# Kernel optimization log

Measured on AMD Instinct MI355X. Metric: run time of the kernel, lower is better.

The kernel has to match this reference:

```python
import jax, jax.numpy as jnp
import numpy as np

DIM_MODEL = 1024
HEADS = 16
DIM_PER_HEAD = DIM_MODEL // HEADS


def setup_inputs() -> dict:
    key = jax.random.key(0)
    k0, k1, k2, k3, k4 = jax.random.split(key, 5)
    x = jax.random.normal(k0, (2, 2048, DIM_MODEL), dtype=jnp.float32)
    # combined_linear: dim_model -> 3*dim_model (torch Linear: y = x @ W.T + b)
    s_in = 1.0 / np.sqrt(DIM_MODEL)
    W_qkv = jax.random.uniform(k1, (3 * DIM_MODEL, DIM_MODEL), minval=-s_in, maxval=s_in, dtype=jnp.float32)
    b_qkv = jax.random.uniform(k2, (3 * DIM_MODEL,), minval=-s_in, maxval=s_in, dtype=jnp.float32)
    W_out = jax.random.uniform(k3, (DIM_MODEL, DIM_MODEL), minval=-s_in, maxval=s_in, dtype=jnp.float32)
    b_out = jax.random.uniform(k4, (DIM_MODEL,), minval=-s_in, maxval=s_in, dtype=jnp.float32)
    return {"x": x, "W_qkv": W_qkv, "b_qkv": b_qkv, "W_out": W_out, "b_out": b_out}


def reference(x, W_qkv, b_qkv, W_out, b_out):
    B, S, D = x.shape
    H, Dh = HEADS, DIM_PER_HEAD
    qkv = x @ W_qkv.T + b_qkv  # [B, S, 3D]
    q, k, v = jnp.split(qkv, 3, axis=2)
    # [B, H, S, Dh]
    q = q.reshape(B, S, H, Dh).transpose(0, 2, 1, 3)
    k = k.reshape(B, S, H, Dh).transpose(0, 2, 1, 3)
    v = v.reshape(B, S, H, Dh).transpose(0, 2, 1, 3)
    scores = jnp.einsum('bhqd,bhkd->bhqk', q, k) / jnp.sqrt(jnp.float32(Dh))
    causal = jnp.tril(jnp.ones((S, S), dtype=bool))
    scores = jnp.where(causal[None, None, :, :], scores, -jnp.inf)
    p_attn = jax.nn.softmax(scores, axis=-1)
    out = jnp.einsum('bhqk,bhkd->bhqd', p_attn, v)
    out = out.transpose(0, 2, 1, 3).reshape(B, S, D)
    return out @ W_out.T + b_out
```

## Files before the change

kernel.cpp:

```cpp
#include <hip/hip_runtime.h>
#include <cstdint>

typedef __attribute__((ext_vector_type(8))) __bf16 bf16x8;
typedef __attribute__((ext_vector_type(4))) float f32x4;
typedef __attribute__((ext_vector_type(8))) short short8;
typedef __attribute__((ext_vector_type(4))) float float4v;
typedef __attribute__((ext_vector_type(4))) unsigned uint4v;
typedef __attribute__((ext_vector_type(4))) unsigned short ushort4v;

__device__ __forceinline__ unsigned short f2bf(float f) {
    unsigned u = __builtin_bit_cast(unsigned, f);
    u += 0x7fffu + ((u >> 16) & 1u);
    return (unsigned short)(u >> 16);
}
__device__ __forceinline__ float bf2f(unsigned short s) {
    return __builtin_bit_cast(float, (unsigned)s << 16);
}
__device__ __forceinline__ f32x4 mfma_bf16(bf16x8 a, bf16x8 b, f32x4 c) {
    return __builtin_amdgcn_mfma_f32_16x16x32_bf16(a, b, c, 0, 0, 0);
}
__device__ __forceinline__ unsigned pkbf(float lo, float hi) {
    unsigned r;
    asm("v_cvt_pk_bf16_f32 %0, %1, %2" : "=v"(r) : "v"(lo), "v"(hi));
    return r;
}

#define GLD16(g, l)                                                                     \
    __builtin_amdgcn_global_load_lds((const __attribute__((address_space(1))) void*)(g), \
                                     (__attribute__((address_space(3))) void*)(l), 16, 0, 0)

__global__ void __launch_bounds__(256) cvt_f32_bf16(const float* __restrict__ src,
                                                    unsigned short* __restrict__ dst, int n8) {
    const int stride = gridDim.x * blockDim.x;
    for (int i = blockIdx.x * blockDim.x + threadIdx.x; i < n8; i += stride) {
        const float4v* s = (const float4v*)(src + (size_t)i * 8);
        float4v v0 = s[0], v1 = s[1];
        short8 o;
        o[0] = (short)f2bf(v0[0]); o[1] = (short)f2bf(v0[1]);
        o[2] = (short)f2bf(v0[2]); o[3] = (short)f2bf(v0[3]);
        o[4] = (short)f2bf(v1[0]); o[5] = (short)f2bf(v1[1]);
        o[6] = (short)f2bf(v1[2]); o[7] = (short)f2bf(v1[3]);
        *(short8*)(dst + (size_t)i * 8) = o;
    }
}

template <int MODE>
__global__ void __launch_bounds__(256) gemm_bt(const unsigned short* __restrict__ A,
                                               const unsigned short* __restrict__ B,
                                               const float* __restrict__ bias,
                                               void* __restrict__ C,
                                               unsigned short* __restrict__ vT,
                                               int M, int N, int K) {
    __shared__ __attribute__((aligned(16))) unsigned short As[2][128 * 32];
    __shared__ __attribute__((aligned(16))) unsigned short Bs[2][128 * 32];
    const int tid = threadIdx.x;
    const int w = tid >> 6, lane = tid & 63;
    const int a = lane & 15, g = lane >> 4;
    const int m0 = blockIdx.y * 128, n0 = blockIdx.x * 128;
    const int wr = (w >> 1) * 64, wc = (w & 1) * 64;

    f32x4 acc[4][4];
#pragma unroll
    for (int i = 0; i < 4; i++)
#pragma unroll
        for (int j = 0; j < 4; j++) acc[i][j] = (f32x4)(0.0f);

    const int r0 = tid >> 2;
    const int c0 = (tid & 3) * 8;
    const unsigned short* gA0 = A + (size_t)(m0 + r0) * K + c0;
    const unsigned short* gA1 = A + (size_t)(m0 + 64 + r0) * K + c0;
    const unsigned short* gB0 = B + (size_t)(n0 + r0) * K + c0;
    const unsigned short* gB1 = B + (size_t)(n0 + 64 + r0) * K + c0;

#define GSTAGE(buf_, k0_)                                               \
    {                                                                   \
        char* la_ = (char*)&As[buf_][0] + w * 1024;                     \
        char* lb_ = (char*)&Bs[buf_][0] + w * 1024;                     \
        GLD16(gA0 + (k0_), la_);                                        \
        GLD16(gA1 + (k0_), la_ + 4096);                                 \
        GLD16(gB0 + (k0_), lb_);                                        \
        GLD16(gB1 + (k0_), lb_ + 4096);                                 \
    }

    GSTAGE(0, 0);
    __syncthreads();

    int cur = 0;
    for (int k0 = 0; k0 < K; k0 += 32) {
        if (k0 + 32 < K) GSTAGE(cur ^ 1, k0 + 32);

        bf16x8 af[4], bfr[4];
#pragma unroll
        for (int i = 0; i < 4; i++) {
            af[i]  = *(const bf16x8*)&As[cur][(wr + i * 16 + a) * 32 + g * 8];
            bfr[i] = *(const bf16x8*)&Bs[cur][(wc + i * 16 + a) * 32 + g * 8];
        }
#pragma unroll
        for (int i = 0; i < 4; i++)
#pragma unroll
            for (int j = 0; j < 4; j++) acc[i][j] = mfma_bf16(af[i], bfr[j], acc[i][j]);

        __syncthreads();
        cur ^= 1;
    }
#undef GSTAGE

#pragma unroll
    for (int j = 0; j < 4; j++) {
        const int col = n0 + wc + j * 16 + a;
        const float bv = bias[col];
        if (MODE == 0) {
            float* Cf = (float*)C;
#pragma unroll
            for (int i = 0; i < 4; i++)
#pragma unroll
                for (int jr = 0; jr < 4; jr++) {
                    const int row = m0 + wr + i * 16 + g * 4 + jr;
                    Cf[(size_t)row * N + col] = acc[i][j][jr] + bv;
                }
        } else if (n0 < 2048) {
            unsigned short* Cb = (unsigned short*)C;
#pragma unroll
            for (int i = 0; i < 4; i++)
#pragma unroll
                for (int jr = 0; jr < 4; jr++) {
                    const int row = m0 + wr + i * 16 + g * 4 + jr;
                    Cb[(size_t)row * 2048 + col] = f2bf(acc[i][j][jr] + bv);
                }
        } else {
            const int vd = col - 2048;
            const int hh = vd >> 6, dd = vd & 63;
#pragma unroll
            for (int i = 0; i < 4; i++) {
                const int token0 = m0 + wr + i * 16 + g * 4;
                const int bb = token0 >> 11, kl = token0 & 2047;
                ushort4v st;
#pragma unroll
                for (int jr = 0; jr < 4; jr++) st[jr] = f2bf(acc[i][j][jr] + bv);
                *(ushort4v*)(vT + ((size_t)((bb << 4) + hh) * 64 + dd) * 2048 + kl) = st;
            }
        }
    }
}


#define QKT_LDS(p, kvb)                                                 \
    {                                                                   \
        _Pragma("unroll") for (int nf_ = 0; nf_ < 4; nf_++) {           \
            const int r_ = srow + ((nf_ & 2) << 4) + ((nf_ & 1) << 2);  \
            const bf16x8 ka_ = *(const bf16x8*)&(kvb)[r_ * 64 + offKA]; \
            const bf16x8 kc_ = *(const bf16x8*)&(kvb)[r_ * 64 + offKB]; \
            f32x4 acc_ = (f32x4)(0.0f);                                 \
            acc_ = mfma_bf16(ka_, qf[0], acc_);                         \
            acc_ = mfma_bf16(kc_, qf[1], acc_);                         \
            p[nf_] = acc_;                                              \
        }                                                               \
    }

#define DIAG_MASK(p, qs_, k0_)                                          \
    {                                                                   \
        _Pragma("unroll") for (int nf_ = 0; nf_ < 4; nf_++) {           \
            const int kb_ = (k0_) + ((nf_ & 2) << 4) + ((nf_ & 1) << 2) + 8 * g; \
            _Pragma("unroll") for (int e_ = 0; e_ < 4; e_++)            \
                if (kb_ + e_ > (qs_)) p[nf_][e_] = -1e30f;              \
        }                                                               \
    }

#define SOFTMAX_PACK(p, m_, l_, of_, pf0, pf1)                          \
    {                                                                   \
        float x0 = fmaxf(fmaxf(p[0][0], p[0][1]), fmaxf(p[0][2], p[0][3])); \
        float x1 = fmaxf(fmaxf(p[1][0], p[1][1]), fmaxf(p[1][2], p[1][3])); \
        float x2 = fmaxf(fmaxf(p[2][0], p[2][1]), fmaxf(p[2][2], p[2][3])); \
        float x3 = fmaxf(fmaxf(p[3][0], p[3][1]), fmaxf(p[3][2], p[3][3])); \
        float mx = fmaxf(fmaxf(x0, x1), fmaxf(x2, x3));                 \
        mx = fmaxf(mx, __shfl_xor(mx, 16));                             \
        mx = fmaxf(mx, __shfl_xor(mx, 32));                             \
        if (!__all(mx <= m_ + 8.0f)) {                                  \
            const float mn_ = fmaxf(m_, mx);                            \
            const float al_ = __builtin_amdgcn_exp2f(m_ - mn_);         \
            l_ *= al_;                                                  \
            _Pragma("unroll") for (int d_ = 0; d_ < 4; d_++) of_[d_] = of_[d_] * al_; \
            m_ = mn_;                                                   \
        }                                                               \
        float rs_ = 0.0f;                                               \
        _Pragma("unroll") for (int nf_ = 0; nf_ < 4; nf_++)             \
            _Pragma("unroll") for (int e_ = 0; e_ < 4; e_++) {          \
                p[nf_][e_] = __builtin_amdgcn_exp2f(p[nf_][e_] - m_);   \
                rs_ += p[nf_][e_];                                      \
            }                                                           \
        l_ += rs_;                                                      \
        uint4v u0_, u1_;                                                \
        u0_[0] = pkbf(p[0][0], p[0][1]); u0_[1] = pkbf(p[0][2], p[0][3]); \
        u0_[2] = pkbf(p[1][0], p[1][1]); u0_[3] = pkbf(p[1][2], p[1][3]); \
        u1_[0] = pkbf(p[2][0], p[2][1]); u1_[1] = pkbf(p[2][2], p[2][3]); \
        u1_[2] = pkbf(p[3][0], p[3][1]); u1_[3] = pkbf(p[3][2], p[3][3]); \
        pf0 = __builtin_bit_cast(bf16x8, u0_);                          \
        pf1 = __builtin_bit_cast(bf16x8, u1_);                          \
    }

#define PV_LDS(of_, pf0, pf1, vb)                                       \
    {                                                                   \
        _Pragma("unroll") for (int df_ = 0; df_ < 4; df_++) {           \
            const bf16x8 va_ = *(const bf16x8*)&(vb)[(df_ * 16 + n) * 64 + offVA]; \
            const bf16x8 vc_ = *(const bf16x8*)&(vb)[(df_ * 16 + n) * 64 + offVB]; \
            of_[df_] = mfma_bf16(va_, pf0, of_[df_]);                   \
            of_[df_] = mfma_bf16(vc_, pf1, of_[df_]);                   \
        }                                                               \
    }

#define STAGE(bf_, t_)                                                  \
    {                                                                   \
        const size_t ko_ = (size_t)(t_) * 64 * LDQ;                     \
        const size_t vo_ = (size_t)(t_) * 64;                           \
        char* db_ = (char*)&KV[bf_][0] + w * 1024;                      \
        GLD16(sK0 + ko_, db_);                                          \
        GLD16(sV0 + vo_, db_ + 8192);                                   \
    }

__global__ void __launch_bounds__(512) attn_fwd(const unsigned short* __restrict__ qk,
                                                const unsigned short* __restrict__ vT,
                                                unsigned short* __restrict__ o) {
    constexpr int SL = 2048, DH = 64, LDQ = 2048;
    constexpr float GAMMA = 0.18033688011112042f;
    const int bh = blockIdx.x & 31;
    const int pr = 15 - (blockIdx.x >> 5);
    const int b = bh >> 4, h = bh & 15;
    const int tid = threadIdx.x;
    const int w = tid >> 6, lane = tid & 63;
    const int n = lane & 15, g = lane >> 4;

    __shared__ __attribute__((aligned(16))) unsigned short KV[2][8192];

    const int myqt = 2 * pr + (w >> 2);
    const int qs = myqt * 64 + (w & 3) * 16 + n;
    const int nt = 2 * pr + 2;

    bf16x8 qf[2];
    {
        const unsigned short* qp = qk + (size_t)(b * SL + qs) * LDQ + h * DH + g * 8;
        short8 la = *(const short8*)qp, lb = *(const short8*)(qp + 32);
        short8 s0, s1;
#pragma unroll
        for (int e = 0; e < 8; e++) {
            s0[e] = (short)f2bf(bf2f((unsigned short)la[e]) * GAMMA);
            s1[e] = (short)f2bf(bf2f((unsigned short)lb[e]) * GAMMA);
        }
        qf[0] = __builtin_bit_cast(bf16x8, s0);
        qf[1] = __builtin_bit_cast(bf16x8, s1);
    }

    const int r0s = tid >> 3, u0s = tid & 7;
    const int xrs = (r0s & 3) | (((r0s >> 3) & 1) << 2);
    const int cs = ((u0s ^ xrs) << 3);
    const unsigned short* sK0 = qk + (size_t)(b * SL + r0s) * LDQ + 1024 + h * DH + cs;
    const unsigned short* sV0 = vT + (size_t)bh * DH * SL + (size_t)r0s * SL + cs;

    const int srow = 8 * (n >> 2) + (n & 3);
    const int xrq = (n & 3) | (((n >> 2) & 1) << 2);
    const int offKA = ((g ^ xrq) << 3);
    const int offKB = offKA ^ 32;
    const int xrv = (n & 3) | (((n >> 3) & 1) << 2);
    const int offVA = ((g ^ xrv) << 3);
    const int offVB = offVA ^ 32;

    f32x4 of[4];
#pragma unroll
    for (int i = 0; i < 4; i++) of[i] = (f32x4)(0.0f);
    float m_i = -1e30f, l_i = 0.0f;

    STAGE(0, 0);
    __syncthreads();

    for (int t = 0; t < nt; ++t) {
        const unsigned short* kvb = &KV[t & 1][0];
        if (t + 1 < nt) STAGE((t & 1) ^ 1, t + 1);

        f32x4 p[4];
        QKT_LDS(p, kvb);
        if (t >= myqt) DIAG_MASK(p, qs, t * 64);
        bf16x8 f0, f1;
        SOFTMAX_PACK(p, m_i, l_i, of, f0, f1);
        PV_LDS(of, f0, f1, (kvb + 4096));

        __syncthreads();
    }

    float rl = l_i;
    rl += __shfl_xor(rl, 16);
    rl += __shfl_xor(rl, 32);
    const float inv = 1.0f / rl;
    unsigned short* op = o + (size_t)(b * SL + qs) * 1024 + h * DH + 4 * g;
#pragma unroll
    for (int df = 0; df < 4; df++) {
        ushort4v st;
#pragma unroll
        for (int r = 0; r < 4; r++) st[r] = f2bf(of[df][r] * inv);
        *(ushort4v*)(op + df * 16) = st;
    }
}

extern "C" void kernel_launch(void* const* d_in, const int* in_sizes, int n_in,
                              void* d_out, int out_size, void* d_ws, size_t ws_size,
                              hipStream_t stream) {
    (void)in_sizes; (void)n_in; (void)out_size; (void)ws_size;
    const float* x    = (const float*)d_in[0];
    const float* Wqkv = (const float*)d_in[1];
    const float* bqkv = (const float*)d_in[2];
    const float* Wout = (const float*)d_in[3];
    const float* bout = (const float*)d_in[4];
    float* out = (float*)d_out;

    const int BS = 2, SL = 2048, DM = 1024;
    const int M = BS * SL;
    const int N1 = 3 * DM;
    const int K = DM;

    char* ws = (char*)d_ws;
    unsigned short* x_bf    = (unsigned short*)(ws);
    unsigned short* wqkv_bf = (unsigned short*)(ws + (8u << 20));
    unsigned short* wout_bf = (unsigned short*)(ws + (14u << 20));
    unsigned short* qkbuf   = (unsigned short*)(ws + (16u << 20));
    unsigned short* vTbuf   = (unsigned short*)(ws + (32u << 20));
    unsigned short* attn_o  = (unsigned short*)(ws + (40u << 20));

    cvt_f32_bf16<<<2048, 256, 0, stream>>>(x, x_bf, M * K / 8);
    cvt_f32_bf16<<<1536, 256, 0, stream>>>(Wqkv, wqkv_bf, N1 * K / 8);
    cvt_f32_bf16<<<512, 256, 0, stream>>>(Wout, wout_bf, DM * DM / 8);

    gemm_bt<1><<<dim3(N1 / 128, M / 128), 256, 0, stream>>>(x_bf, wqkv_bf, bqkv, qkbuf, vTbuf, M, N1, K);

    attn_fwd<<<dim3(512), 512, 0, stream>>>(qkbuf, vTbuf, attn_o);

    gemm_bt<0><<<dim3(DM / 128, M / 128), 256, 0, stream>>>(attn_o, wout_bf, bout, out, nullptr, M, DM, K);
}
```

Measured before the change: 113.6 us.

## Process 128-key tiles with 128-query blocks in causal attention kernel

The attention kernel now gives each block 128 queries (one 16-row slice per wave) and iterates over 128-key K/V tiles instead of 64. This halves the number of loop iterations and __syncthreads barriers and doubles the work per staged LDS buffer. The block scheduling order becomes an interleave of long and short query blocks, and launch bounds request 4 blocks per CU. In exchange it uses twice the shared memory per block (64 KB) and more registers for the larger score tile. Causal masking now runs only on the final tile, where that tile is partly masked for most queries.

```diff
diff --git a/kernel.cpp b/kernel.cpp
--- a/kernel.cpp
+++ b/kernel.cpp
@@ -144,96 +144,34 @@
 }
 
 
-#define QKT_LDS(p, kvb)                                                 \
-    {                                                                   \
-        _Pragma("unroll") for (int nf_ = 0; nf_ < 4; nf_++) {           \
-            const int r_ = srow + ((nf_ & 2) << 4) + ((nf_ & 1) << 2);  \
-            const bf16x8 ka_ = *(const bf16x8*)&(kvb)[r_ * 64 + offKA]; \
-            const bf16x8 kc_ = *(const bf16x8*)&(kvb)[r_ * 64 + offKB]; \
-            f32x4 acc_ = (f32x4)(0.0f);                                 \
-            acc_ = mfma_bf16(ka_, qf[0], acc_);                         \
-            acc_ = mfma_bf16(kc_, qf[1], acc_);                         \
-            p[nf_] = acc_;                                              \
-        }                                                               \
-    }
-
-#define DIAG_MASK(p, qs_, k0_)                                          \
-    {                                                                   \
-        _Pragma("unroll") for (int nf_ = 0; nf_ < 4; nf_++) {           \
-            const int kb_ = (k0_) + ((nf_ & 2) << 4) + ((nf_ & 1) << 2) + 8 * g; \
-            _Pragma("unroll") for (int e_ = 0; e_ < 4; e_++)            \
-                if (kb_ + e_ > (qs_)) p[nf_][e_] = -1e30f;              \
-        }                                                               \
-    }
-
-#define SOFTMAX_PACK(p, m_, l_, of_, pf0, pf1)                          \
-    {                                                                   \
-        float x0 = fmaxf(fmaxf(p[0][0], p[0][1]), fmaxf(p[0][2], p[0][3])); \
-        float x1 = fmaxf(fmaxf(p[1][0], p[1][1]), fmaxf(p[1][2], p[1][3])); \
-        float x2 = fmaxf(fmaxf(p[2][0], p[2][1]), fmaxf(p[2][2], p[2][3])); \
-        float x3 = fmaxf(fmaxf(p[3][0], p[3][1]), fmaxf(p[3][2], p[3][3])); \
-        float mx = fmaxf(fmaxf(x0, x1), fmaxf(x2, x3));                 \
-        mx = fmaxf(mx, __shfl_xor(mx, 16));                             \
-        mx = fmaxf(mx, __shfl_xor(mx, 32));                             \
-        if (!__all(mx <= m_ + 8.0f)) {                                  \
-            const float mn_ = fmaxf(m_, mx);                            \
-            const float al_ = __builtin_amdgcn_exp2f(m_ - mn_);         \
-            l_ *= al_;                                                  \
-            _Pragma("unroll") for (int d_ = 0; d_ < 4; d_++) of_[d_] = of_[d_] * al_; \
-            m_ = mn_;                                                   \
-        }                                                               \
-        float rs_ = 0.0f;                                               \
-        _Pragma("unroll") for (int nf_ = 0; nf_ < 4; nf_++)             \
-            _Pragma("unroll") for (int e_ = 0; e_ < 4; e_++) {          \
-                p[nf_][e_] = __builtin_amdgcn_exp2f(p[nf_][e_] - m_);   \
-                rs_ += p[nf_][e_];                                      \
-            }                                                           \
-        l_ += rs_;                                                      \
-        uint4v u0_, u1_;                                                \
-        u0_[0] = pkbf(p[0][0], p[0][1]); u0_[1] = pkbf(p[0][2], p[0][3]); \
-        u0_[2] = pkbf(p[1][0], p[1][1]); u0_[3] = pkbf(p[1][2], p[1][3]); \
-        u1_[0] = pkbf(p[2][0], p[2][1]); u1_[1] = pkbf(p[2][2], p[2][3]); \
-        u1_[2] = pkbf(p[3][0], p[3][1]); u1_[3] = pkbf(p[3][2], p[3][3]); \
-        pf0 = __builtin_bit_cast(bf16x8, u0_);                          \
-        pf1 = __builtin_bit_cast(bf16x8, u1_);                          \
-    }
-
-#define PV_LDS(of_, pf0, pf1, vb)                                       \
-    {                                                                   \
-        _Pragma("unroll") for (int df_ = 0; df_ < 4; df_++) {           \
-            const bf16x8 va_ = *(const bf16x8*)&(vb)[(df_ * 16 + n) * 64 + offVA]; \
-            const bf16x8 vc_ = *(const bf16x8*)&(vb)[(df_ * 16 + n) * 64 + offVB]; \
-            of_[df_] = mfma_bf16(va_, pf0, of_[df_]);                   \
-            of_[df_] = mfma_bf16(vc_, pf1, of_[df_]);                   \
-        }                                                               \
-    }
-
 #define STAGE(bf_, t_)                                                  \
     {                                                                   \
-        const size_t ko_ = (size_t)(t_) * 64 * LDQ;                     \
-        const size_t vo_ = (size_t)(t_) * 64;                           \
+        const size_t ko_ = (size_t)(t_) * 128 * LDQ;                    \
+        const size_t vo_ = (size_t)(t_) * 128;                          \
         char* db_ = (char*)&KV[bf_][0] + w * 1024;                      \
         GLD16(sK0 + ko_, db_);                                          \
-        GLD16(sV0 + vo_, db_ + 8192);                                   \
-    }
-
-__global__ void __launch_bounds__(512) attn_fwd(const unsigned short* __restrict__ qk,
-                                                const unsigned short* __restrict__ vT,
-                                                unsigned short* __restrict__ o) {
+        GLD16(sK1 + ko_, db_ + 8192);                                   \
+        GLD16(sV0 + vo_, db_ + 16384);                                  \
+        GLD16(sV1 + vo_, db_ + 24576);                                  \
+    }
+
+__global__ void __launch_bounds__(512, 4) attn_fwd(const unsigned short* __restrict__ qk,
+                                                   const unsigned short* __restrict__ vT,
+                                                   unsigned short* __restrict__ o) {
     constexpr int SL = 2048, DH = 64, LDQ = 2048;
     constexpr float GAMMA = 0.18033688011112042f;
     const int bh = blockIdx.x & 31;
-    const int pr = 15 - (blockIdx.x >> 5);
+    const int s = blockIdx.x >> 5;
+    const int qb = (s < 8) ? 15 - s : s - 8;
     const int b = bh >> 4, h = bh & 15;
     const int tid = threadIdx.x;
     const int w = tid >> 6, lane = tid & 63;
     const int n = lane & 15, g = lane >> 4;
 
-    __shared__ __attribute__((aligned(16))) unsigned short KV[2][8192];
-
-    const int myqt = 2 * pr + (w >> 2);
-    const int qs = myqt * 64 + (w & 3) * 16 + n;
-    const int nt = 2 * pr + 2;
+    __shared__ __attribute__((aligned(16))) unsigned short KV[2][16384];
+
+    const int qs = qb * 128 + w * 16 + n;
+    const int nt = qb + 1;
 
     bf16x8 qf[2];
     {
@@ -249,19 +187,23 @@
         qf[1] = __builtin_bit_cast(bf16x8, s1);
     }
 
-    const int r0s = tid >> 3, u0s = tid & 7;
-    const int xrs = (r0s & 3) | (((r0s >> 3) & 1) << 2);
-    const int cs = ((u0s ^ xrs) << 3);
-    const unsigned short* sK0 = qk + (size_t)(b * SL + r0s) * LDQ + 1024 + h * DH + cs;
-    const unsigned short* sV0 = vT + (size_t)bh * DH * SL + (size_t)r0s * SL + cs;
+    const int rK = tid >> 3;
+    const int xrK = (rK & 3) | (((rK >> 3) & 1) << 2);
+    const int csK = (((tid & 7) ^ xrK) << 3);
+    const unsigned short* sK0 = qk + (size_t)(b * SL + rK) * LDQ + 1024 + h * DH + csK;
+    const unsigned short* sK1 = sK0 + (size_t)64 * LDQ;
+    const int dV = tid >> 4;
+    const int csV = (((tid & 15) ^ (dV & 7)) << 3);
+    const unsigned short* sV0 = vT + (size_t)bh * DH * SL + (size_t)dV * SL + csV;
+    const unsigned short* sV1 = sV0 + (size_t)32 * SL;
 
     const int srow = 8 * (n >> 2) + (n & 3);
     const int xrq = (n & 3) | (((n >> 2) & 1) << 2);
-    const int offKA = ((g ^ xrq) << 3);
-    const int offKB = offKA ^ 32;
-    const int xrv = (n & 3) | (((n >> 3) & 1) << 2);
-    const int offVA = ((g ^ xrv) << 3);
-    const int offVB = offVA ^ 32;
+    const int offK0 = ((g ^ xrq) << 3);
+    const int offK1 = offK0 ^ 32;
+    int offV[4];
+#pragma unroll
+    for (int kc = 0; kc < 4; kc++) offV[kc] = (((4 * kc + g) ^ (n & 7)) << 3);
 
     f32x4 of[4];
 #pragma unroll
@@ -275,12 +217,76 @@
         const unsigned short* kvb = &KV[t & 1][0];
         if (t + 1 < nt) STAGE((t & 1) ^ 1, t + 1);
 
-        f32x4 p[4];
-        QKT_LDS(p, kvb);
-        if (t >= myqt) DIAG_MASK(p, qs, t * 64);
-        bf16x8 f0, f1;
-        SOFTMAX_PACK(p, m_i, l_i, of, f0, f1);
-        PV_LDS(of, f0, f1, (kvb + 4096));
+        f32x4 p[8];
+#pragma unroll
+        for (int f = 0; f < 8; f++) {
+            const int r_ = srow + ((f >> 1) << 5) + ((f & 1) << 2);
+            const bf16x8 ka_ = *(const bf16x8*)&kvb[r_ * 64 + offK0];
+            const bf16x8 kc_ = *(const bf16x8*)&kvb[r_ * 64 + offK1];
+            f32x4 acc_ = (f32x4)(0.0f);
+            acc_ = mfma_bf16(ka_, qf[0], acc_);
+            acc_ = mfma_bf16(kc_, qf[1], acc_);
+            p[f] = acc_;
+        }
+
+        if (t == nt - 1) {
+            const int k0 = t * 128;
+#pragma unroll
+            for (int f = 0; f < 8; f++) {
+                const int kb_ = k0 + ((f >> 1) << 5) + ((f & 1) << 2) + 8 * g;
+#pragma unroll
+                for (int e = 0; e < 4; e++)
+                    if (kb_ + e > qs) p[f][e] = -1e30f;
+            }
+        }
+
+        float mx = -1e30f;
+#pragma unroll
+        for (int f = 0; f < 8; f++) {
+            const float a_ = fmaxf(fmaxf(p[f][0], p[f][1]), fmaxf(p[f][2], p[f][3]));
+            mx = fmaxf(mx, a_);
+        }
+        mx = fmaxf(mx, __shfl_xor(mx, 16));
+        mx = fmaxf(mx, __shfl_xor(mx, 32));
+        if (!__all(mx <= m_i + 8.0f)) {
+            const float mn_ = fmaxf(m_i, mx);
+            const float al_ = __builtin_amdgcn_exp2f(m_i - mn_);
+            l_i *= al_;
+#pragma unroll
+            for (int d_ = 0; d_ < 4; d_++) of[d_] = of[d_] * al_;
+            m_i = mn_;
+        }
+        float rs = 0.0f;
+#pragma unroll
+        for (int f = 0; f < 8; f++)
+#pragma unroll
+            for (int e = 0; e < 4; e++) {
+                p[f][e] = __builtin_amdgcn_exp2f(p[f][e] - m_i);
+                rs += p[f][e];
+            }
+        l_i += rs;
+
+        bf16x8 pf[4];
+#pragma unroll
+        for (int kc = 0; kc < 4; kc++) {
+            uint4v u_;
+            u_[0] = pkbf(p[2 * kc][0], p[2 * kc][1]);
+            u_[1] = pkbf(p[2 * kc][2], p[2 * kc][3]);
+            u_[2] = pkbf(p[2 * kc + 1][0], p[2 * kc + 1][1]);
+            u_[3] = pkbf(p[2 * kc + 1][2], p[2 * kc + 1][3]);
+            pf[kc] = __builtin_bit_cast(bf16x8, u_);
+        }
+
+        const unsigned short* vb = kvb + 8192;
+#pragma unroll
+        for (int df = 0; df < 4; df++) {
+            const int vrow = (df * 16 + n) * 128;
+#pragma unroll
+            for (int kc = 0; kc < 4; kc++) {
+                const bf16x8 va_ = *(const bf16x8*)&vb[vrow + offV[kc]];
+                of[df] = mfma_bf16(va_, pf[kc], of[df]);
+            }
+        }
 
         __syncthreads();
     }
```

Measured after the change: 108.2 us, median of 2. 1.05x faster.
